# Kernel tuning notes

Hardware: AMD Instinct MI355X
Metric: run time of the kernel (lower is better)

The kernel has to match this reference:

```python
import jax, jax.numpy as jnp
import numpy as np

N_HEAD = 16
ROPE_BASE = 10000.0


def setup_inputs() -> dict:
    key = jax.random.key(0)
    k1, k2, k3 = jax.random.split(key, 3)
    B, N, C = 2, 2048, 2048
    x = jax.random.normal(k1, (B, N, C), dtype=jnp.float32)
    position_ids = jnp.tile(jnp.arange(N, dtype=jnp.int64)[None, :], (B, 1))
    # torch nn.Linear(d, 3d) weight is [3d, d]; we store the transposed [d, 3d] for x @ W
    Wqkv = jax.random.normal(k2, (C, 3 * C), dtype=jnp.float32) * (C ** -0.5)
    Wproj = jax.random.normal(k3, (C, C), dtype=jnp.float32) * (C ** -0.5)
    return {"x": x, "position_ids": position_ids, "Wqkv": Wqkv, "Wproj": Wproj}


def _rotate_half(t):
    d = t.shape[-1] // 2
    return jnp.concatenate([-t[..., d:], t[..., :d]], axis=-1)


def reference(x, position_ids, Wqkv, Wproj):
    B, N, C = x.shape
    H = N_HEAD
    hd = C // H
    scale = hd ** -0.5

    # fused QKV projection -> [3, B, H, N, hd]
    qkv = (x @ Wqkv).reshape(B, N, 3, H, hd).transpose(2, 0, 3, 1, 4)
    q, k, v = qkv[0], qkv[1], qkv[2]

    # RoPE (computed in fp32 as in the original)
    inv_freq = 1.0 / (ROPE_BASE ** (jnp.arange(0, hd, 2, dtype=jnp.float32) / hd))
    freqs = position_ids.astype(jnp.float32)[:, :, None] * inv_freq[None, None, :]  # [B, N, hd/2]
    emb = jnp.concatenate([freqs, freqs], axis=-1)                                  # [B, N, hd]
    cos = jnp.cos(emb)[:, None, :, :].astype(x.dtype)  # [B, 1, N, hd]
    sin = jnp.sin(emb)[:, None, :, :].astype(x.dtype)
    q = q * cos + _rotate_half(q) * sin
    k = k * cos + _rotate_half(k) * sin

    # causal SDPA
    scores = jnp.einsum('bhqd,bhkd->bhqk', q, k) * scale
    causal = jnp.tril(jnp.ones((N, N), dtype=bool))
    scores = jnp.where(causal[None, None, :, :], scores, jnp.finfo(scores.dtype).min)
    attn = jax.nn.softmax(scores, axis=-1)
    out = jnp.einsum('bhqk,bhkd->bhqd', attn, v)

    out = out.transpose(0, 2, 1, 3).reshape(B, N, C)
    return out @ Wproj
```

## Files before the change

### kernel.cpp

```cpp
#include <hip/hip_runtime.h>
#include <stdint.h>

#define DEV __device__ __forceinline__

typedef __attribute__((ext_vector_type(8))) short short8;
typedef __attribute__((ext_vector_type(8))) unsigned short ushort8;
typedef __attribute__((ext_vector_type(4))) float f32x4;
typedef __attribute__((ext_vector_type(16))) float f32x16;
typedef __attribute__((ext_vector_type(2))) unsigned int uint2v;

DEV unsigned short f2bf(float f) {
  union { float f; uint32_t u; } v; v.f = f;
  uint32_t u = v.u;
  u += 0x7FFFu + ((u >> 16) & 1);
  return (unsigned short)(u >> 16);
}
DEV float bf2f(unsigned short s) {
  union { uint32_t u; float f; } v; v.u = ((uint32_t)s) << 16;
  return v.f;
}
DEV float exp2_fast(float x) {
  float r; asm("v_exp_f32 %0, %1" : "=v"(r) : "v"(x)); return r;
}
DEV uint32_t cvt_pk_bf16(float lo, float hi) {
  uint32_t r; asm("v_cvt_pk_bf16_f32 %0, %1, %2" : "=v"(r) : "v"(lo), "v"(hi)); return r;
}

DEV void async_ld16(void* lds, const void* g) {
  __builtin_amdgcn_global_load_lds(
      (const __attribute__((address_space(1))) unsigned int*)g,
      (__attribute__((address_space(3))) unsigned int*)lds, 16, 0, 0);
}

__global__ __launch_bounds__(256) void cast_bf16_kernel(
    const float* __restrict__ in, unsigned short* __restrict__ out, int n) {
  int i = (blockIdx.x * 256 + threadIdx.x) * 4;
  if (i >= n) return;
  f32x4 v = *(const f32x4*)(in + i);
  union { unsigned short u[4]; uint2v v2; } o;
#pragma unroll
  for (int j = 0; j < 4; ++j) o.u[j] = f2bf(v[j]);
  *(uint2v*)(out + i) = o.v2;
}

__global__ __launch_bounds__(256) void transpose_cast_kernel(
    const float* __restrict__ in, unsigned short* __restrict__ out, int R, int C) {
  __shared__ float tile[32][33];
  const int c0 = blockIdx.x * 32, r0 = blockIdx.y * 32;
  const int tx = threadIdx.x & 31, ty = threadIdx.x >> 5;
#pragma unroll
  for (int i = 0; i < 32; i += 8)
    tile[ty + i][tx] = in[(size_t)(r0 + ty + i) * C + c0 + tx];
  __syncthreads();
#pragma unroll
  for (int i = 0; i < 32; i += 8)
    out[(size_t)(c0 + ty + i) * R + r0 + tx] = f2bf(tile[tx][ty + i]);
}

template <int OUT_BF16>
__global__ __launch_bounds__(512, 2) void gemm_bt(
    const unsigned short* __restrict__ A, const unsigned short* __restrict__ Bt,
    void* __restrict__ Cout, int M, int Nn, int K) {
  __shared__ unsigned short As[2][256 * 64];
  __shared__ unsigned short Bs[2][128 * 64];
  const int t = threadIdx.x;
  const int lane = t & 63, w = t >> 6;
  const int wr = (w >> 1) * 64;
  const int wc = (w & 1) * 64;
  const int brow = blockIdx.y * 256, bcol = blockIdx.x * 128;
  const int l15 = lane & 15, lk = lane >> 4;
  const int p = l15 & 7;

  f32x4 acc[4][4] = {};

  auto stage = [&](int buf, int ktile) {
    const int koff = ktile * 64;
#pragma unroll
    for (int j = 0; j < 4; ++j) {
      const int slot = j * 512 + t;
      const int row = slot >> 3, ch = slot & 7;
      const int sc = ch ^ (row & 7);
      async_ld16(&As[buf][slot * 8], A + (size_t)(brow + row) * K + koff + sc * 8);
    }
#pragma unroll
    for (int j = 0; j < 2; ++j) {
      const int slot = j * 512 + t;
      const int row = slot >> 3, ch = slot & 7;
      const int sc = ch ^ (row & 7);
      async_ld16(&Bs[buf][slot * 8], Bt + (size_t)(bcol + row) * K + koff + sc * 8);
    }
  };

  const int NT = K / 64;
  stage(0, 0);
  stage(1, 1);

  for (int kt = 0; kt < NT; ++kt) {
    const int cur = kt & 1;
    if (kt == NT - 1) { asm volatile("s_waitcnt vmcnt(0)" ::: "memory"); }
    else              { asm volatile("s_waitcnt vmcnt(6)" ::: "memory"); }
    __builtin_amdgcn_sched_barrier(0);
    __builtin_amdgcn_s_barrier();

    short8 af0[4], af1[4], bf0[4], bf1[4];
#pragma unroll
    for (int m = 0; m < 4; ++m) {
      const int row = wr + m * 16 + l15;
      af0[m] = *(const short8*)&As[cur][row * 64 + (lk ^ p) * 8];
      af1[m] = *(const short8*)&As[cur][row * 64 + ((4 + lk) ^ p) * 8];
    }
#pragma unroll
    for (int n = 0; n < 4; ++n) {
      const int row = wc + n * 16 + l15;
      bf0[n] = *(const short8*)&Bs[cur][row * 64 + (lk ^ p) * 8];
      bf1[n] = *(const short8*)&Bs[cur][row * 64 + ((4 + lk) ^ p) * 8];
    }

    __builtin_amdgcn_s_setprio(1);
#pragma unroll
    for (int m = 0; m < 4; ++m)
#pragma unroll
      for (int n = 0; n < 4; ++n)
        acc[m][n] = __builtin_amdgcn_mfma_f32_16x16x32_bf16(af0[m], bf0[n], acc[m][n], 0, 0, 0);
    __builtin_amdgcn_s_setprio(0);

    asm volatile("s_waitcnt lgkmcnt(0)" ::: "memory");
    __builtin_amdgcn_sched_barrier(0);
    __builtin_amdgcn_s_barrier();
    if (kt + 2 < NT) stage(cur, kt + 2);

    __builtin_amdgcn_s_setprio(1);
#pragma unroll
    for (int m = 0; m < 4; ++m)
#pragma unroll
      for (int n = 0; n < 4; ++n)
        acc[m][n] = __builtin_amdgcn_mfma_f32_16x16x32_bf16(af1[m], bf1[n], acc[m][n], 0, 0, 0);
    __builtin_amdgcn_s_setprio(0);
  }

#pragma unroll
  for (int m = 0; m < 4; ++m)
#pragma unroll
    for (int n = 0; n < 4; ++n)
#pragma unroll
      for (int j = 0; j < 4; ++j) {
        const int row = brow + wr + m * 16 + lk * 4 + j;
        const int col = bcol + wc + n * 16 + l15;
        if (OUT_BF16)
          ((unsigned short*)Cout)[(size_t)row * Nn + col] = f2bf(acc[m][n][j]);
        else
          ((float*)Cout)[(size_t)row * Nn + col] = acc[m][n][j];
      }
}

#define QSCALE 0.12751743f
__global__ __launch_bounds__(256) void rope_pack(
    const unsigned short* __restrict__ Y, const int* __restrict__ pos,
    unsigned short* __restrict__ Qb, unsigned short* __restrict__ Kb,
    unsigned short* __restrict__ Vt, int N) {
  __shared__ unsigned short vt[128 * 32];
  const int bh = blockIdx.x, b = bh >> 4, h = bh & 15;
  const int n0 = blockIdx.y * 32;
  const int t = threadIdx.x;
  const int tok = t >> 3, dp0 = (t & 7) * 8;
  const int n = n0 + tok;
  const float p = (float)pos[b * N + n];
  const size_t yb = (size_t)(b * N + n) * 6144 + h * 128;

  ushort8 qlo = *(const ushort8*)&Y[yb + dp0];
  ushort8 qhi = *(const ushort8*)&Y[yb + dp0 + 64];
  ushort8 klo = *(const ushort8*)&Y[yb + 2048 + dp0];
  ushort8 khi = *(const ushort8*)&Y[yb + 2048 + dp0 + 64];
  ushort8 vlo = *(const ushort8*)&Y[yb + 4096 + dp0];
  ushort8 vhi = *(const ushort8*)&Y[yb + 4096 + dp0 + 64];

  ushort8 oql, oqh, okl, okh;
#pragma unroll
  for (int i = 0; i < 8; ++i) {
    const float d = (float)(dp0 + i);
    const float ang = p * exp2f(d * -0.2076205059304601f);
    const float s = sinf(ang), c = cosf(ang);
    const float ql = bf2f(qlo[i]), qh = bf2f(qhi[i]);
    const float kl = bf2f(klo[i]), kh = bf2f(khi[i]);
    oql[i] = f2bf((ql * c - qh * s) * QSCALE);
    oqh[i] = f2bf((qh * c + ql * s) * QSCALE);
    okl[i] = f2bf(kl * c - kh * s);
    okh[i] = f2bf(kh * c + kl * s);
    vt[(dp0 + i) * 32 + tok] = vlo[i];
    vt[(dp0 + 64 + i) * 32 + tok] = vhi[i];
  }
  const size_t qb = ((size_t)bh * N + n) * 128;
  *(ushort8*)&Qb[qb + dp0] = oql;
  *(ushort8*)&Qb[qb + dp0 + 64] = oqh;
  *(ushort8*)&Kb[qb + dp0] = okl;
  *(ushort8*)&Kb[qb + dp0 + 64] = okh;
  __syncthreads();
  const int d = t >> 1, half = t & 1;
  const size_t vdst = (size_t)bh * 128 * N + (size_t)d * N + n0 + half * 16;
  *(ushort8*)&Vt[vdst]     = *(const ushort8*)&vt[d * 32 + half * 16];
  *(ushort8*)&Vt[vdst + 8] = *(const ushort8*)&vt[d * 32 + half * 16 + 8];
}

__global__ __launch_bounds__(512, 2) void flash_attn8(
    const unsigned short* __restrict__ Qb, const unsigned short* __restrict__ Kb,
    const unsigned short* __restrict__ Vt, unsigned short* __restrict__ Ao, int N) {
  __shared__ unsigned short Ks[2][32 * 128];
  __shared__ unsigned short Vs[2][128 * 32];
  const int t = threadIdx.x, lane = t & 63, w = t >> 6;
  const int bh = blockIdx.x, b = bh >> 4, h = bh & 15;
  const int c = blockIdx.y;
  const int qchunk = (w < 4) ? c : (15 - c);
  const int q0 = qchunk * 128 + (w & 3) * 32;
  const int l31 = lane & 31, hi = lane >> 5;
  const size_t base = (size_t)bh * N * 128;
  const size_t vbase = (size_t)bh * 128 * N;
  const int Twave = q0 >> 5;
  const int Tblk = (15 - c) * 4 + 4;

  const int krow = t >> 4, kch = (t & 15) ^ (krow & 7);
  const int vrow = t >> 2, vch = (t & 3) ^ (vrow & 3);

  auto stage = [&](int tt, int buf) {
    const int kv0 = tt * 32;
    async_ld16(&Ks[buf][t * 8], Kb + base + (size_t)(kv0 + krow) * 128 + kch * 8);
    async_ld16(&Vs[buf][t * 8], Vt + vbase + (size_t)vrow * N + kv0 + vch * 8);
  };

  short8 qf[8];
#pragma unroll
  for (int s = 0; s < 8; ++s)
    qf[s] = *(const short8*)&Qb[base + (size_t)(q0 + l31) * 128 + s * 16 + hi * 8];

  f32x16 acc0 = {}, acc1 = {}, acc2 = {}, acc3 = {};
  float m_run = -1e30f, l_run = 0.f;

  stage(0, 0);
  stage(1, 1);

  for (int tt = 0; tt < Tblk; ++tt) {
    const int cur = tt & 1;
    if (tt < Tblk - 1) { asm volatile("s_waitcnt vmcnt(2)" ::: "memory"); }
    else               { asm volatile("s_waitcnt vmcnt(0)" ::: "memory"); }
    __builtin_amdgcn_sched_barrier(0);
    __builtin_amdgcn_s_barrier();

    if (tt <= Twave) {
      const int kv0 = tt * 32;
      const bool masked = (tt == Twave);

      short8 kf[8];
#pragma unroll
      for (int s = 0; s < 8; ++s)
        kf[s] = *(const short8*)&Ks[cur][l31 * 128 + ((2 * s + hi) ^ (l31 & 7)) * 8];
      short8 vf[8];
#pragma unroll
      for (int cc = 0; cc < 2; ++cc)
#pragma unroll
        for (int dblk = 0; dblk < 4; ++dblk) {
          const int row = dblk * 32 + l31;
          vf[cc * 4 + dblk] = *(const short8*)&Vs[cur][row * 32 + ((2 * cc + hi) ^ (row & 3)) * 8];
        }

      f32x16 st = {};
      __builtin_amdgcn_s_setprio(1);
#pragma unroll
      for (int s = 0; s < 8; ++s)
        st = __builtin_amdgcn_mfma_f32_32x32x16_bf16(kf[s], qf[s], st, 0, 0, 0);
      __builtin_amdgcn_s_setprio(0);

      if (masked) {
        const int qg = q0 + l31;
#pragma unroll
        for (int r = 0; r < 16; ++r) {
          const int kvg = kv0 + (r & 3) + 8 * ((r >> 2) & 1) + 16 * (r >> 3) + 4 * hi;
          st[r] = (kvg > qg) ? -1e30f : st[r];
        }
      }
      float a0 = fmaxf(st[0], st[1]),  a1 = fmaxf(st[2], st[3]),
            a2 = fmaxf(st[4], st[5]),  a3 = fmaxf(st[6], st[7]),
            a4 = fmaxf(st[8], st[9]),  a5 = fmaxf(st[10], st[11]),
            a6 = fmaxf(st[12], st[13]), a7 = fmaxf(st[14], st[15]);
      a0 = fmaxf(a0, a1); a2 = fmaxf(a2, a3); a4 = fmaxf(a4, a5); a6 = fmaxf(a6, a7);
      a0 = fmaxf(a0, a2); a4 = fmaxf(a4, a6);
      float mt = fmaxf(a0, a4);
      mt = fmaxf(mt, __shfl_xor(mt, 32));

      float m_new = fmaxf(m_run, mt);
      const bool defer = __all(mt - m_run <= 8.f);
      if (defer) {
        m_new = m_run;
      } else {
        const float alpha = exp2_fast(m_run - m_new);
        l_run *= alpha;
#pragma unroll
        for (int r = 0; r < 16; ++r) {
          acc0[r] *= alpha; acc1[r] *= alpha; acc2[r] *= alpha; acc3[r] *= alpha;
        }
      }
      m_run = m_new;

#pragma unroll
      for (int r = 0; r < 16; ++r) st[r] = exp2_fast(st[r] - m_new);
      float s0 = (st[0] + st[1]) + (st[2] + st[3]), s1 = (st[4] + st[5]) + (st[6] + st[7]);
      float s2 = (st[8] + st[9]) + (st[10] + st[11]), s3 = (st[12] + st[13]) + (st[14] + st[15]);
      float lsum = (s0 + s1) + (s2 + s3);
      lsum += __shfl_xor(lsum, 32);
      l_run += lsum;

      short8 pB0, pB1;
#pragma unroll
      for (int cc = 0; cc < 2; ++cc) {
        const int o = cc * 8;
        const uint32_t P01 = cvt_pk_bf16(st[o + 0], st[o + 1]);
        const uint32_t P23 = cvt_pk_bf16(st[o + 2], st[o + 3]);
        const uint32_t P45 = cvt_pk_bf16(st[o + 4], st[o + 5]);
        const uint32_t P67 = cvt_pk_bf16(st[o + 6], st[o + 7]);
        const uint32_t S01 = (uint32_t)__shfl_xor((int)P01, 32);
        const uint32_t S23 = (uint32_t)__shfl_xor((int)P23, 32);
        const uint32_t S45 = (uint32_t)__shfl_xor((int)P45, 32);
        const uint32_t S67 = (uint32_t)__shfl_xor((int)P67, 32);
        union { uint32_t ww[4]; short8 s8; } u;
        u.ww[0] = hi ? S45 : P01;
        u.ww[1] = hi ? S67 : P23;
        u.ww[2] = hi ? P45 : S01;
        u.ww[3] = hi ? P67 : S23;
        if (cc == 0) pB0 = u.s8; else pB1 = u.s8;
      }

      __builtin_amdgcn_s_setprio(1);
      acc0 = __builtin_amdgcn_mfma_f32_32x32x16_bf16(vf[0], pB0, acc0, 0, 0, 0);
      acc1 = __builtin_amdgcn_mfma_f32_32x32x16_bf16(vf[1], pB0, acc1, 0, 0, 0);
      acc2 = __builtin_amdgcn_mfma_f32_32x32x16_bf16(vf[2], pB0, acc2, 0, 0, 0);
      acc3 = __builtin_amdgcn_mfma_f32_32x32x16_bf16(vf[3], pB0, acc3, 0, 0, 0);
      acc0 = __builtin_amdgcn_mfma_f32_32x32x16_bf16(vf[4], pB1, acc0, 0, 0, 0);
      acc1 = __builtin_amdgcn_mfma_f32_32x32x16_bf16(vf[5], pB1, acc1, 0, 0, 0);
      acc2 = __builtin_amdgcn_mfma_f32_32x32x16_bf16(vf[6], pB1, acc2, 0, 0, 0);
      acc3 = __builtin_amdgcn_mfma_f32_32x32x16_bf16(vf[7], pB1, acc3, 0, 0, 0);
      __builtin_amdgcn_s_setprio(0);
    }

    asm volatile("s_waitcnt lgkmcnt(0)" ::: "memory");
    __builtin_amdgcn_sched_barrier(0);
    __builtin_amdgcn_s_barrier();
    if (tt + 2 < Tblk) stage(tt + 2, cur);
  }

  const float inv = 1.f / l_run;
  const size_t orow = (size_t)(b * N + q0 + l31) * 2048 + h * 128;
#pragma unroll
  for (int r = 0; r < 16; r += 2) {
    const int doff = (r & 3) + 8 * ((r >> 2) & 1) + 16 * (r >> 3) + 4 * hi;
    *(uint32_t*)&Ao[orow + 0  + doff] = cvt_pk_bf16(acc0[r] * inv, acc0[r + 1] * inv);
    *(uint32_t*)&Ao[orow + 32 + doff] = cvt_pk_bf16(acc1[r] * inv, acc1[r + 1] * inv);
    *(uint32_t*)&Ao[orow + 64 + doff] = cvt_pk_bf16(acc2[r] * inv, acc2[r + 1] * inv);
    *(uint32_t*)&Ao[orow + 96 + doff] = cvt_pk_bf16(acc3[r] * inv, acc3[r + 1] * inv);
  }
}

extern "C" void kernel_launch(void* const* d_in, const int* in_sizes, int n_in,
                              void* d_out, int out_size, void* d_ws, size_t ws_size,
                              hipStream_t stream) {
  const float* x      = (const float*)d_in[0];
  const int*   pos    = (const int*)d_in[1];
  const float* Wqkv   = (const float*)d_in[2];
  const float* Wproj  = (const float*)d_in[3];
  float* out = (float*)d_out;

  const int N = 2048, C = 2048;
  const int M = 2 * N;

  char* ws = (char*)d_ws;
  unsigned short* Xb      = (unsigned short*)(ws + 0);
  unsigned short* Wqkv_t  = (unsigned short*)(ws + 16777216);
  unsigned short* Wproj_t = (unsigned short*)(ws + 41943040);
  unsigned short* Y       = (unsigned short*)(ws + 50331648);
  unsigned short* Qb      = (unsigned short*)(ws + 100663296);
  unsigned short* Kb      = (unsigned short*)(ws + 117440512);
  unsigned short* Vt      = (unsigned short*)(ws + 134217728);
  unsigned short* Ao = Xb;

  cast_bf16_kernel<<<(M * C) / 1024, 256, 0, stream>>>(x, Xb, M * C);
  transpose_cast_kernel<<<dim3(3 * C / 32, C / 32), 256, 0, stream>>>(Wqkv, Wqkv_t, C, 3 * C);
  transpose_cast_kernel<<<dim3(C / 32, C / 32), 256, 0, stream>>>(Wproj, Wproj_t, C, C);
  gemm_bt<1><<<dim3(3 * C / 128, M / 256), 512, 0, stream>>>(Xb, Wqkv_t, Y, M, 3 * C, C);
  rope_pack<<<dim3(32, N / 32), 256, 0, stream>>>(Y, pos, Qb, Kb, Vt, N);
  flash_attn8<<<dim3(32, 8), 512, 0, stream>>>(Qb, Kb, Vt, Ao, N);
  gemm_bt<0><<<dim3(C / 128, M / 256), 512, 0, stream>>>(Ao, Wproj_t, out, M, C, C);
}
```

Measured before the change: 293.9 us.

## Triple-buffer GEMM shared tiles and interleave async prefetch with MFMA phases

Moves the bf16 GEMM from double to triple LDS buffering, so the prefetch for tile kt+2 can go into a third buffer. That removes the second per-iteration block barrier. The global-to-LDS loads for the next tile are split into parts issued around the two MFMA half-steps, and the LDS fragment reads are likewise split per half, which should overlap memory traffic with compute better. LDS use rises to about 144KB per block, which limits occupancy to one block per CU and adds modulo-3 buffer indexing.

```diff
diff --git a/kernel.cpp b/kernel.cpp
--- a/kernel.cpp
+++ b/kernel.cpp
@@ -61,8 +61,8 @@
 __global__ __launch_bounds__(512, 2) void gemm_bt(
     const unsigned short* __restrict__ A, const unsigned short* __restrict__ Bt,
     void* __restrict__ Cout, int M, int Nn, int K) {
-  __shared__ unsigned short As[2][256 * 64];
-  __shared__ unsigned short Bs[2][128 * 64];
+  __shared__ unsigned short As[3][256 * 64];
+  __shared__ unsigned short Bs[3][128 * 64];
   const int t = threadIdx.x;
   const int lane = t & 63, w = t >> 6;
   const int wr = (w >> 1) * 64;
@@ -73,17 +73,20 @@
 
   f32x4 acc[4][4] = {};
 
-  auto stage = [&](int buf, int ktile) {
+  auto stageA = [&](int buf, int ktile, int j0, int j1) {
     const int koff = ktile * 64;
 #pragma unroll
-    for (int j = 0; j < 4; ++j) {
+    for (int j = j0; j < j1; ++j) {
       const int slot = j * 512 + t;
       const int row = slot >> 3, ch = slot & 7;
       const int sc = ch ^ (row & 7);
       async_ld16(&As[buf][slot * 8], A + (size_t)(brow + row) * K + koff + sc * 8);
     }
-#pragma unroll
-    for (int j = 0; j < 2; ++j) {
+  };
+  auto stageB = [&](int buf, int ktile, int j0, int j1) {
+    const int koff = ktile * 64;
+#pragma unroll
+    for (int j = j0; j < j1; ++j) {
       const int slot = j * 512 + t;
       const int row = slot >> 3, ch = slot & 7;
       const int sc = ch ^ (row & 7);
@@ -92,30 +95,29 @@
   };
 
   const int NT = K / 64;
-  stage(0, 0);
-  stage(1, 1);
+  stageA(0, 0, 0, 4); stageB(0, 0, 0, 2);
+  stageA(1, 1, 0, 4); stageB(1, 1, 0, 2);
 
   for (int kt = 0; kt < NT; ++kt) {
-    const int cur = kt & 1;
+    const int cur = kt % 3;
+    const int nxt = (kt + 2) % 3;
+    const bool pre = (kt + 2 < NT);
     if (kt == NT - 1) { asm volatile("s_waitcnt vmcnt(0)" ::: "memory"); }
     else              { asm volatile("s_waitcnt vmcnt(6)" ::: "memory"); }
     __builtin_amdgcn_sched_barrier(0);
     __builtin_amdgcn_s_barrier();
-
-    short8 af0[4], af1[4], bf0[4], bf1[4];
-#pragma unroll
-    for (int m = 0; m < 4; ++m) {
-      const int row = wr + m * 16 + l15;
-      af0[m] = *(const short8*)&As[cur][row * 64 + (lk ^ p) * 8];
-      af1[m] = *(const short8*)&As[cur][row * 64 + ((4 + lk) ^ p) * 8];
-    }
-#pragma unroll
-    for (int n = 0; n < 4; ++n) {
-      const int row = wc + n * 16 + l15;
-      bf0[n] = *(const short8*)&Bs[cur][row * 64 + (lk ^ p) * 8];
-      bf1[n] = *(const short8*)&Bs[cur][row * 64 + ((4 + lk) ^ p) * 8];
-    }
-
+    __builtin_amdgcn_sched_barrier(0);
+
+    if (pre) { stageA(nxt, kt + 2, 0, 3); }
+    short8 af0[4], bf0[4];
+#pragma unroll
+    for (int m = 0; m < 4; ++m)
+      af0[m] = *(const short8*)&As[cur][(wr + m * 16 + l15) * 64 + (lk ^ p) * 8];
+#pragma unroll
+    for (int n = 0; n < 4; ++n)
+      bf0[n] = *(const short8*)&Bs[cur][(wc + n * 16 + l15) * 64 + (lk ^ p) * 8];
+    asm volatile("s_waitcnt lgkmcnt(0)" ::: "memory");
+    __builtin_amdgcn_sched_barrier(0);
     __builtin_amdgcn_s_setprio(1);
 #pragma unroll
     for (int m = 0; m < 4; ++m)
@@ -124,11 +126,16 @@
         acc[m][n] = __builtin_amdgcn_mfma_f32_16x16x32_bf16(af0[m], bf0[n], acc[m][n], 0, 0, 0);
     __builtin_amdgcn_s_setprio(0);
 
+    if (pre) { stageA(nxt, kt + 2, 3, 4); stageB(nxt, kt + 2, 0, 2); }
+    short8 af1[4], bf1[4];
+#pragma unroll
+    for (int m = 0; m < 4; ++m)
+      af1[m] = *(const short8*)&As[cur][(wr + m * 16 + l15) * 64 + ((4 + lk) ^ p) * 8];
+#pragma unroll
+    for (int n = 0; n < 4; ++n)
+      bf1[n] = *(const short8*)&Bs[cur][(wc + n * 16 + l15) * 64 + ((4 + lk) ^ p) * 8];
     asm volatile("s_waitcnt lgkmcnt(0)" ::: "memory");
     __builtin_amdgcn_sched_barrier(0);
-    __builtin_amdgcn_s_barrier();
-    if (kt + 2 < NT) stage(cur, kt + 2);
-
     __builtin_amdgcn_s_setprio(1);
 #pragma unroll
     for (int m = 0; m < 4; ++m)
```

Result: slower. 337.3 us (+14.8%).

## Split flash attention blocks into single query chunks with four waves

Applied to the files above, without the earlier changes.

The attention kernel drops the 8-wave blocks that paired a short and a long causal query chunk for a 4-wave block handling one 128-row chunk. The grid doubles to 512 blocks and is ordered so the longest chunks launch first. Each thread now issues two async loads per K and V tile, and the vmcnt wait is adjusted to match. This removes the wasted K/V staging of the old pairing, where the short-chunk waves sat idle for most iterations, and lets the longest-first order balance load across CUs. In exchange each block amortises its K/V loads over fewer waves, so per-FLOP load traffic is higher.

```diff
diff --git a/kernel.cpp b/kernel.cpp
--- a/kernel.cpp
+++ b/kernel.cpp
@@ -201,29 +201,36 @@
   *(ushort8*)&Vt[vdst + 8] = *(const ushort8*)&vt[d * 32 + half * 16 + 8];
 }
 
-__global__ __launch_bounds__(512, 2) void flash_attn8(
+__global__ __launch_bounds__(256, 2) void flash_attn4(
     const unsigned short* __restrict__ Qb, const unsigned short* __restrict__ Kb,
     const unsigned short* __restrict__ Vt, unsigned short* __restrict__ Ao, int N) {
   __shared__ unsigned short Ks[2][32 * 128];
   __shared__ unsigned short Vs[2][128 * 32];
   const int t = threadIdx.x, lane = t & 63, w = t >> 6;
   const int bh = blockIdx.x, b = bh >> 4, h = bh & 15;
-  const int c = blockIdx.y;
-  const int qchunk = (w < 4) ? c : (15 - c);
-  const int q0 = qchunk * 128 + (w & 3) * 32;
+  const int y = blockIdx.y;
+  const int cc = (y < 8) ? (15 - y) : (y - 8);
+  const int q0 = cc * 128 + w * 32;
   const int l31 = lane & 31, hi = lane >> 5;
   const size_t base = (size_t)bh * N * 128;
   const size_t vbase = (size_t)bh * 128 * N;
-  const int Twave = q0 >> 5;
-  const int Tblk = (15 - c) * 4 + 4;
-
-  const int krow = t >> 4, kch = (t & 15) ^ (krow & 7);
-  const int vrow = t >> 2, vch = (t & 3) ^ (vrow & 3);
+  const int Twave = 4 * cc + w;
+  const int Tblk = 4 * cc + 4;
 
   auto stage = [&](int tt, int buf) {
     const int kv0 = tt * 32;
-    async_ld16(&Ks[buf][t * 8], Kb + base + (size_t)(kv0 + krow) * 128 + kch * 8);
-    async_ld16(&Vs[buf][t * 8], Vt + vbase + (size_t)vrow * N + kv0 + vch * 8);
+#pragma unroll
+    for (int j = 0; j < 2; ++j) {
+      const int slot = j * 256 + t;
+      const int krow = slot >> 4, kch = (slot & 15) ^ (krow & 7);
+      async_ld16(&Ks[buf][slot * 8], Kb + base + (size_t)(kv0 + krow) * 128 + kch * 8);
+    }
+#pragma unroll
+    for (int j = 0; j < 2; ++j) {
+      const int slot = j * 256 + t;
+      const int vrow = slot >> 2, vch = (slot & 3) ^ (vrow & 3);
+      async_ld16(&Vs[buf][slot * 8], Vt + vbase + (size_t)vrow * N + kv0 + vch * 8);
+    }
   };
 
   short8 qf[8];
@@ -239,7 +246,7 @@
 
   for (int tt = 0; tt < Tblk; ++tt) {
     const int cur = tt & 1;
-    if (tt < Tblk - 1) { asm volatile("s_waitcnt vmcnt(2)" ::: "memory"); }
+    if (tt < Tblk - 1) { asm volatile("s_waitcnt vmcnt(4)" ::: "memory"); }
     else               { asm volatile("s_waitcnt vmcnt(0)" ::: "memory"); }
     __builtin_amdgcn_sched_barrier(0);
     __builtin_amdgcn_s_barrier();
@@ -254,11 +261,11 @@
         kf[s] = *(const short8*)&Ks[cur][l31 * 128 + ((2 * s + hi) ^ (l31 & 7)) * 8];
       short8 vf[8];
 #pragma unroll
-      for (int cc = 0; cc < 2; ++cc)
+      for (int c2 = 0; c2 < 2; ++c2)
 #pragma unroll
         for (int dblk = 0; dblk < 4; ++dblk) {
           const int row = dblk * 32 + l31;
-          vf[cc * 4 + dblk] = *(const short8*)&Vs[cur][row * 32 + ((2 * cc + hi) ^ (row & 3)) * 8];
+          vf[c2 * 4 + dblk] = *(const short8*)&Vs[cur][row * 32 + ((2 * c2 + hi) ^ (row & 3)) * 8];
         }
 
       f32x16 st = {};
@@ -309,8 +316,8 @@
 
       short8 pB0, pB1;
 #pragma unroll
-      for (int cc = 0; cc < 2; ++cc) {
-        const int o = cc * 8;
+      for (int c2 = 0; c2 < 2; ++c2) {
+        const int o = c2 * 8;
         const uint32_t P01 = cvt_pk_bf16(st[o + 0], st[o + 1]);
         const uint32_t P23 = cvt_pk_bf16(st[o + 2], st[o + 3]);
         const uint32_t P45 = cvt_pk_bf16(st[o + 4], st[o + 5]);
@@ -324,7 +331,7 @@
         u.ww[1] = hi ? S67 : P23;
         u.ww[2] = hi ? P45 : S01;
         u.ww[3] = hi ? P67 : S23;
-        if (cc == 0) pB0 = u.s8; else pB1 = u.s8;
+        if (c2 == 0) pB0 = u.s8; else pB1 = u.s8;
       }
 
       __builtin_amdgcn_s_setprio(1);
@@ -384,6 +391,6 @@
   transpose_cast_kernel<<<dim3(C / 32, C / 32), 256, 0, stream>>>(Wproj, Wproj_t, C, C);
   gemm_bt<1><<<dim3(3 * C / 128, M / 256), 512, 0, stream>>>(Xb, Wqkv_t, Y, M, 3 * C, C);
   rope_pack<<<dim3(32, N / 32), 256, 0, stream>>>(Y, pos, Qb, Kb, Vt, N);
-  flash_attn8<<<dim3(32, 8), 512, 0, stream>>>(Qb, Kb, Vt, Ao, N);
+  flash_attn4<<<dim3(32, 16), 256, 0, stream>>>(Qb, Kb, Vt, Ao, N);
   gemm_bt<0><<<dim3(C / 128, M / 256), 512, 0, stream>>>(Ao, Wproj_t, out, M, C, C);
 }
```

After: 291.3 us. Within noise of the previous version (-0.9%).
